# Performance work log

Measured on AMD Instinct MI355X. Metric: run time of the kernel, lower is better.

Reference implementation:

```python
import jax, jax.numpy as jnp
import numpy as np

BN_EPS = 1e-5
NUM_SUBSET = 3


def conv1x1(x, w, b):
    # x: [N, C, T, V], w: [O, C], b: [O]  (1x1 Conv2d)
    return jnp.einsum('nctv,oc->notv', x, w) + b[:, None, None]


def setup_inputs() -> dict:
    key = jax.random.key(0)
    ks = jax.random.split(key, 8)
    N, C, T, V = 64, 64, 300, 25
    IC = 16  # inter_c = out_channels // coff_embedding
    O = 64
    inp = {
        'x': jax.random.normal(ks[0], (N, C, T, V), dtype=jnp.float32),
        'A': jax.random.uniform(ks[1], (NUM_SUBSET, V, V), dtype=jnp.float32),
        'graph_attn': jnp.ones((NUM_SUBSET, V, V), dtype=jnp.float32),
        'g_w': jax.random.normal(ks[2], (NUM_SUBSET, O, C), dtype=jnp.float32) * 0.05,
        'g_b': jnp.zeros((NUM_SUBSET, O), dtype=jnp.float32),
        'a_w': jax.random.normal(ks[3], (NUM_SUBSET, IC, C), dtype=jnp.float32) * 0.05,
        'a_b': jnp.zeros((NUM_SUBSET, IC), dtype=jnp.float32),
        'b_w': jax.random.normal(ks[4], (NUM_SUBSET, IC, C), dtype=jnp.float32) * 0.05,
        'b_b': jnp.zeros((NUM_SUBSET, IC), dtype=jnp.float32),
        'bn_gamma': jnp.ones((O,), dtype=jnp.float32),
        'bn_beta': jnp.zeros((O,), dtype=jnp.float32),
        'bn_mean': jnp.zeros((O,), dtype=jnp.float32),
        'bn_var': jnp.ones((O,), dtype=jnp.float32),
    }
    return inp


def reference(x, A, graph_attn, g_w, g_b, a_w, a_b, b_w, b_b,
              bn_gamma, bn_beta, bn_mean, bn_var):
    N, C, T, V = x.shape
    IC = a_w.shape[1]
    A_tot = A + graph_attn  # [3, V, V]
    x_flat = x.reshape(N, C * T, V)
    hidden = None
    for i in range(NUM_SUBSET):
        # a_conv -> permute(0,3,1,2) -> [N, V, IC*T]
        A1 = conv1x1(x, a_w[i], a_b[i]).transpose(0, 3, 1, 2).reshape(N, V, IC * T)
        # b_conv -> [N, IC*T, V]
        A2 = conv1x1(x, b_w[i], b_b[i]).reshape(N, IC * T, V)
        attn = jax.nn.softmax(jnp.matmul(A1, A2) / (IC * T), axis=-2)  # [N, V, V], softmax over rows
        attn = attn + A_tot[i]
        z = jnp.matmul(x_flat, attn).reshape(N, C, T, V)
        z = conv1x1(z, g_w[i], g_b[i])
        hidden = z if hidden is None else hidden + z
    # BatchNorm2d in eval mode over channel dim
    inv = jax.lax.rsqrt(bn_var + BN_EPS)
    hidden = (hidden - bn_mean[:, None, None]) * (inv * bn_gamma)[:, None, None] + bn_beta[:, None, None]
    # in_channels == out_channels -> identity residual
    hidden = hidden + x
    return jax.nn.relu(hidden)
```

## Files before the change

kernel.cpp:

```cpp
#include <hip/hip_runtime.h>


#define NB 64
#define CB 64
#define TB 300
#define VB 25

typedef unsigned int uint32;
typedef unsigned short ushort16;
typedef __attribute__((ext_vector_type(8))) short short8;
typedef __attribute__((ext_vector_type(4))) float f32x4;
typedef __attribute__((ext_vector_type(16))) float f32x16;

__device__ __forceinline__ ushort16 f2bf(float f) {
    uint32 u = __float_as_uint(f);
    u = u + 0x7FFFu + ((u >> 16) & 1u);
    return (ushort16)(u >> 16);
}
__device__ __forceinline__ float bf2f(ushort16 h) {
    return __uint_as_float(((uint32)h) << 16);
}
__device__ __forceinline__ uint32 packbf2(float a, float b) {
    return (uint32)f2bf(a) | ((uint32)f2bf(b) << 16);
}

__global__ __launch_bounds__(256) void k1_attn_logits_mfma(
    const float* __restrict__ x, const float* __restrict__ a_w,
    const float* __restrict__ a_b, const float* __restrict__ b_w,
    const float* __restrict__ b_b, float* __restrict__ Mb)
{
    __shared__ ushort16 ws[96 * 64];
    __shared__ ushort16 xT[112 * 64];
    __shared__ ushort16 abT[192 * 64];
    __shared__ float    bias[96];

    const int tid   = threadIdx.x;
    const int n     = blockIdx.x / 25;
    const int chunk = blockIdx.x % 25;
    const float* xn = x + n * (CB * TB * VB);

    for (int idx = tid; idx < 6144; idx += 256) {
        int r = idx >> 6, c = idx & 63;
        float v = (r < 48) ? a_w[r * 64 + c] : b_w[(r - 48) * 64 + c];
        ws[r * 64 + ((((c >> 3) + r) & 7) << 3) + (c & 7)] = f2bf(v);
    }
    for (int idx = tid; idx < 96; idx += 256)
        bias[idx] = (idx < 48) ? a_b[idx] : b_b[idx - 48];

    const int w    = tid >> 6;
    const int lane = tid & 63;
    const int l15  = lane & 15;
    const int q    = lane >> 4;
    const int hi   = lane >> 5;
    const int v32  = lane & 31;

    f32x16 acc[3];
    #pragma unroll
    for (int i = 0; i < 3; ++i)
        #pragma unroll
        for (int r = 0; r < 16; ++r) acc[i][r] = 0.f;
    const f32x4 zf = (f32x4){0.f, 0.f, 0.f, 0.f};

    for (int s = 0; s < 3; ++s) {
        __syncthreads();
        const float* xs0 = xn + (chunk * 12 + s * 4) * 25;
        for (int idx = tid; idx < 1600; idx += 256) {
            int c = idx / 25, j = idx % 25;
            float4 v4 = *(const float4*)(xs0 + c * 7500 + j * 4);
            int tv0 = j * 4;
            #pragma unroll
            for (int e = 0; e < 4; ++e) {
                int tv = tv0 + e;
                float fv = (e == 0) ? v4.x : (e == 1) ? v4.y : (e == 2) ? v4.z : v4.w;
                xT[tv * 64 + ((((c >> 3) + tv) & 7) << 3) + (c & 7)] = f2bf(fv);
            }
        }
        __syncthreads();
        for (int tile = w; tile < 42; tile += 4) {
            int rt = tile / 7, ct = tile % 7;
            int r  = rt * 16 + l15;
            int tv = ct * 16 + l15;
            f32x4 d = zf;
            #pragma unroll
            for (int ss = 0; ss < 2; ++ss) {
                int kb = ss * 4 + q;
                short8 af = *(const short8*)&ws[r * 64 + (((kb + r) & 7) << 3)];
                short8 bf = *(const short8*)&xT[tv * 64 + (((kb + tv) & 7) << 3)];
                d = __builtin_amdgcn_mfma_f32_16x16x32_bf16(af, bf, d, 0, 0, 0);
            }
            if (tv < 100) {
                int tl = tv / 25, v = tv % 25;
                int r0 = rt * 16 + q * 4;
                float b0 = bias[r0], b1 = bias[r0 + 1];
                float b2 = bias[r0 + 2], b3 = bias[r0 + 3];
                int kb = tl * 2 + (q >> 1);
                uint32* dst = (uint32*)&abT[(rt * 32 + v) * 64 +
                                            (((kb + v) & 7) << 3) + ((q & 1) << 2)];
                dst[0] = packbf2(d[0] + b0, d[1] + b1);
                dst[1] = packbf2(d[2] + b2, d[3] + b3);
            }
        }
        __syncthreads();
        {
            int kb = w * 2 + hi;
            #pragma unroll
            for (int i = 0; i < 3; ++i) {
                short8 af = *(const short8*)&abT[(i * 32 + v32) * 64 +
                                                 (((kb + v32) & 7) << 3)];
                short8 bf = *(const short8*)&abT[((3 + i) * 32 + v32) * 64 +
                                                 (((kb + v32) & 7) << 3)];
                acc[i] = __builtin_amdgcn_mfma_f32_32x32x16_bf16(af, bf, acc[i], 0, 0, 0);
            }
        }
    }

    float* Ms = (float*)xT;
    __syncthreads();
    for (int idx = tid; idx < 3 * 32 * 33; idx += 256) Ms[idx] = 0.f;
    __syncthreads();
    for (int wv = 0; wv < 4; ++wv) {
        if (w == wv) {
            #pragma unroll
            for (int i = 0; i < 3; ++i)
                #pragma unroll
                for (int r = 0; r < 16; ++r) {
                    int row = (r & 3) + 8 * (r >> 2) + 4 * hi;
                    Ms[i * 1056 + row * 33 + v32] += acc[i][r];
                }
        }
        __syncthreads();
    }
    const float inv = 1.0f / 4800.0f;
    for (int idx = tid; idx < 1875; idx += 256) {
        int i = idx / 625, rem = idx % 625;
        int v1 = rem / 25, v2 = rem % 25;
        atomicAdd(Mb + ((i * NB + n) * 25 + v1) * 25 + v2,
                  Ms[i * 1056 + v1 * 33 + v2] * inv);
    }
}

__global__ __launch_bounds__(256) void k2_softmax_prep(
    const float* __restrict__ Mb, const float* __restrict__ A,
    const float* __restrict__ GA, const float* __restrict__ g_w,
    uint32* __restrict__ atT, uint32* __restrict__ gwb)
{
    int idx = blockIdx.x * 256 + threadIdx.x;
    if (idx < 4800) {
        int v2 = idx % 25, n = (idx / 25) % 64, i = idx / 1600;
        const float* mcol = Mb + ((i * 64 + n) * 25) * 25 + v2;
        float e[25], mx = -1e30f;
        #pragma unroll
        for (int v1 = 0; v1 < 25; ++v1) { e[v1] = mcol[v1 * 25]; mx = fmaxf(mx, e[v1]); }
        float s = 0.f;
        #pragma unroll
        for (int v1 = 0; v1 < 25; ++v1) { e[v1] = __expf(e[v1] - mx); s += e[v1]; }
        float invs = 1.0f / s;
        const float* acol = A + i * 625 + v2;
        const float* gcol = GA + i * 625 + v2;
        float w[25];
        #pragma unroll
        for (int v1 = 0; v1 < 25; ++v1)
            w[v1] = e[v1] * invs + acol[v1 * 25] + gcol[v1 * 25];
        uint32* row = atT + ((i * 64 + n) * 32 + v2) * 16;
        #pragma unroll
        for (int p = 0; p < 12; ++p) row[p] = packbf2(w[2 * p], w[2 * p + 1]);
        row[12] = (uint32)f2bf(w[24]);
        row[13] = 0u; row[14] = 0u; row[15] = 0u;
    } else if (idx < 4800 + 6144) {
        int j = idx - 4800;
        int o = j / 96, kp = j % 96;
        int k0 = 2 * kp;
        int i = k0 >> 6, c = k0 & 63;
        float lo = g_w[(i * 64 + o) * 64 + c];
        float hi = g_w[(i * 64 + o) * 64 + c + 1];
        gwb[o * 96 + kp] = packbf2(lo, hi);
    }
}

__global__ __launch_bounds__(256) void k3_out(
    const float* __restrict__ x, const uint32* __restrict__ atT,
    const ushort16* __restrict__ gwb, const float* __restrict__ g_b,
    const float* __restrict__ bn_g, const float* __restrict__ bn_b,
    const float* __restrict__ bn_m, const float* __restrict__ bn_v,
    float* __restrict__ out)
{
    __shared__ ushort16 xs[64 * 168];
    __shared__ uint32  xa[128 * 36];
    __shared__ uint32  ats[3 * 32 * 20];
    __shared__ float   bsc[64], bsh[64];

    const int tid = threadIdx.x;
    const int n  = blockIdx.x / 60;
    const int t0 = (blockIdx.x % 60) * 5;

    for (int idx = tid; idx < 8000; idx += 256) {
        int c = idx / 125, tv = idx % 125;
        int t = tv / 25, v = tv % 25;
        float g = x[((n * 64 + c) * 300 + t0 + t) * 25 + v];
        xs[c * 168 + t * 32 + v] = f2bf(g);
    }
    for (int idx = tid; idx < 64 * 35; idx += 256) {
        int c = idx / 35, r = idx % 35;
        xs[c * 168 + (r / 7) * 32 + 25 + (r % 7)] = (ushort16)0;
    }
    for (int idx = tid; idx < 1536; idx += 256) {
        int row = idx >> 4, d = idx & 15;
        ats[row * 20 + d] = atT[((row >> 5) * 64 + n) * 512 + (row & 31) * 16 + d];
    }
    for (int idx = tid; idx < 64; idx += 256) {
        float sc = bn_g[idx] * rsqrtf(bn_v[idx] + 1e-5f);
        bsc[idx] = sc;
        bsh[idx] = (g_b[idx] + g_b[64 + idx] + g_b[128 + idx] - bn_m[idx]) * sc + bn_b[idx];
    }
    for (int idx = tid; idx < 3 * 36; idx += 256)
        xa[(125 + idx / 36) * 36 + idx % 36] = 0u;

    const int w    = tid >> 6;
    const int lane = tid & 63;
    const int l15  = lane & 15;
    const int q    = lane >> 4;

    short8 gf[6];
    #pragma unroll
    for (int s = 0; s < 6; ++s)
        gf[s] = *(const short8*)(gwb + ((w * 16 + l15) * 192 + s * 32 + q * 8));

    f32x4 acc[8];
    #pragma unroll
    for (int ct = 0; ct < 8; ++ct) acc[ct] = (f32x4){0.f, 0.f, 0.f, 0.f};
    const f32x4 zf = (f32x4){0.f, 0.f, 0.f, 0.f};

    __syncthreads();

    for (int i = 0; i < 3; ++i) {
        if (i) __syncthreads();
        #pragma unroll
        for (int t = 0; t < 5; ++t) {
            short8 ax = *(const short8*)(xs + (w * 16 + l15) * 168 + t * 32 + q * 8);
            #pragma unroll
            for (int vt = 0; vt < 2; ++vt) {
                short8 bt = *(const short8*)((const ushort16*)ats +
                                             (i * 32 + vt * 16 + l15) * 40 + q * 8);
                f32x4 d = __builtin_amdgcn_mfma_f32_16x16x32_bf16(ax, bt, zf, 0, 0, 0);
                int v2 = vt * 16 + l15;
                if (v2 < 25) {
                    int col = t * 25 + v2;
                    int c0  = w * 16 + q * 4;
                    xa[col * 36 + (c0 >> 1)]     = packbf2(d[0], d[1]);
                    xa[col * 36 + (c0 >> 1) + 1] = packbf2(d[2], d[3]);
                }
            }
        }
        __syncthreads();
        #pragma unroll
        for (int ct = 0; ct < 8; ++ct) {
            #pragma unroll
            for (int s = 0; s < 2; ++s) {
                short8 bfrag = *(const short8*)((const ushort16*)xa +
                                                (ct * 16 + l15) * 72 + s * 32 + q * 8);
                acc[ct] = __builtin_amdgcn_mfma_f32_16x16x32_bf16(
                    gf[i * 2 + s], bfrag, acc[ct], 0, 0, 0);
            }
        }
    }

    const int o0 = w * 16 + q * 4;
    #pragma unroll
    for (int ct = 0; ct < 8; ++ct) {
        int col = ct * 16 + l15;
        if (col < 125) {
            int tl = col / 25;
            int v  = col - tl * 25;
            float* ob = out + (n * 64 + o0) * 7500 + t0 * 25 + col;
            #pragma unroll
            for (int r = 0; r < 4; ++r) {
                int o = o0 + r;
                float xv = bf2f(xs[o * 168 + tl * 32 + v]);
                float h = acc[ct][r] * bsc[o] + bsh[o] + xv;
                ob[r * 7500] = fmaxf(h, 0.f);
            }
        }
    }
}

extern "C" void kernel_launch(void* const* d_in, const int* in_sizes, int n_in,
                              void* d_out, int out_size, void* d_ws, size_t ws_size,
                              hipStream_t stream) {
    const float* x    = (const float*)d_in[0];
    const float* A    = (const float*)d_in[1];
    const float* GA   = (const float*)d_in[2];
    const float* g_w  = (const float*)d_in[3];
    const float* g_b  = (const float*)d_in[4];
    const float* a_w  = (const float*)d_in[5];
    const float* a_b  = (const float*)d_in[6];
    const float* b_w  = (const float*)d_in[7];
    const float* b_b  = (const float*)d_in[8];
    const float* bn_g = (const float*)d_in[9];
    const float* bn_b = (const float*)d_in[10];
    const float* bn_m = (const float*)d_in[11];
    const float* bn_v = (const float*)d_in[12];
    float* out = (float*)d_out;

    float*  Mb  = (float*)d_ws;
    uint32* atT = (uint32*)((char*)d_ws + 480000);
    uint32* gwb = (uint32*)((char*)d_ws + 480000 + 393216);

    hipMemsetAsync(d_ws, 0, 480000, stream);
    k1_attn_logits_mfma<<<dim3(1600), dim3(256), 0, stream>>>(x, a_w, a_b, b_w, b_b, Mb);
    k2_softmax_prep<<<dim3(43), dim3(256), 0, stream>>>(Mb, A, GA, g_w, atT, gwb);
    k3_out<<<dim3(3840), dim3(256), 0, stream>>>(x, atT, (const ushort16*)gwb,
                                                 g_b, bn_g, bn_b, bn_m, bn_v, out);
}
```

Baseline: 370.5 us.

## Split attention-logit MFMA by subset per wave and drop LDS reduction

In k1, each of three waves now owns one subset and accumulates all four time slices itself. Partial results go straight to global memory with atomics, so the LDS staging reduction and its serialized per-wave syncs are gone. The xT swizzle is changed to reduce LDS bank conflicts, and weight loading is vectorized to float2. k2 is restructured into one 64-thread block per (subset, batch) that stages the logits in LDS, plus vectorized g_w packing. One wave in k1 now idles during the logit MFMA phase, and more atomics hit global memory.

```diff
diff --git a/kernel.cpp b/kernel.cpp
--- a/kernel.cpp
+++ b/kernel.cpp
@@ -22,6 +22,10 @@
 }
 __device__ __forceinline__ uint32 packbf2(float a, float b) {
     return (uint32)f2bf(a) | ((uint32)f2bf(b) << 16);
+}
+
+__device__ __forceinline__ int xt_swz(int kb, int tv) {
+    return ((kb + tv + (tv >> 2)) & 7) << 3;
 }
 
 __global__ __launch_bounds__(256) void k1_attn_logits_mfma(
@@ -39,10 +43,13 @@
     const int chunk = blockIdx.x % 25;
     const float* xn = x + n * (CB * TB * VB);
 
-    for (int idx = tid; idx < 6144; idx += 256) {
-        int r = idx >> 6, c = idx & 63;
-        float v = (r < 48) ? a_w[r * 64 + c] : b_w[(r - 48) * 64 + c];
-        ws[r * 64 + ((((c >> 3) + r) & 7) << 3) + (c & 7)] = f2bf(v);
+    for (int idx = tid; idx < 3072; idx += 256) {
+        int r = idx >> 5, cp = idx & 31;
+        int c = cp * 2;
+        float2 v2 = (r < 48) ? *(const float2*)(a_w + r * 64 + c)
+                             : *(const float2*)(b_w + (r - 48) * 64 + c);
+        *(uint32*)&ws[r * 64 + ((((c >> 3) + r) & 7) << 3) + (c & 7)] =
+            packbf2(v2.x, v2.y);
     }
     for (int idx = tid; idx < 96; idx += 256)
         bias[idx] = (idx < 48) ? a_b[idx] : b_b[idx - 48];
@@ -54,11 +61,9 @@
     const int hi   = lane >> 5;
     const int v32  = lane & 31;
 
-    f32x16 acc[3];
+    f32x16 acc;
     #pragma unroll
-    for (int i = 0; i < 3; ++i)
-        #pragma unroll
-        for (int r = 0; r < 16; ++r) acc[i][r] = 0.f;
+    for (int r = 0; r < 16; ++r) acc[r] = 0.f;
     const f32x4 zf = (f32x4){0.f, 0.f, 0.f, 0.f};
 
     for (int s = 0; s < 3; ++s) {
@@ -72,7 +77,7 @@
             for (int e = 0; e < 4; ++e) {
                 int tv = tv0 + e;
                 float fv = (e == 0) ? v4.x : (e == 1) ? v4.y : (e == 2) ? v4.z : v4.w;
-                xT[tv * 64 + ((((c >> 3) + tv) & 7) << 3) + (c & 7)] = f2bf(fv);
+                xT[tv * 64 + xt_swz(c >> 3, tv) + (c & 7)] = f2bf(fv);
             }
         }
         __syncthreads();
@@ -85,7 +90,7 @@
             for (int ss = 0; ss < 2; ++ss) {
                 int kb = ss * 4 + q;
                 short8 af = *(const short8*)&ws[r * 64 + (((kb + r) & 7) << 3)];
-                short8 bf = *(const short8*)&xT[tv * 64 + (((kb + tv) & 7) << 3)];
+                short8 bf = *(const short8*)&xT[tv * 64 + xt_swz(kb, tv)];
                 d = __builtin_amdgcn_mfma_f32_16x16x32_bf16(af, bf, d, 0, 0, 0);
             }
             if (tv < 100) {
@@ -101,79 +106,77 @@
             }
         }
         __syncthreads();
-        {
-            int kb = w * 2 + hi;
-            #pragma unroll
-            for (int i = 0; i < 3; ++i) {
-                short8 af = *(const short8*)&abT[(i * 32 + v32) * 64 +
+        if (w < 3) {
+            #pragma unroll
+            for (int tl = 0; tl < 4; ++tl) {
+                int kb = tl * 2 + hi;
+                short8 af = *(const short8*)&abT[(w * 32 + v32) * 64 +
                                                  (((kb + v32) & 7) << 3)];
-                short8 bf = *(const short8*)&abT[((3 + i) * 32 + v32) * 64 +
+                short8 bf = *(const short8*)&abT[((3 + w) * 32 + v32) * 64 +
                                                  (((kb + v32) & 7) << 3)];
-                acc[i] = __builtin_amdgcn_mfma_f32_32x32x16_bf16(af, bf, acc[i], 0, 0, 0);
-            }
-        }
-    }
-
-    float* Ms = (float*)xT;
-    __syncthreads();
-    for (int idx = tid; idx < 3 * 32 * 33; idx += 256) Ms[idx] = 0.f;
-    __syncthreads();
-    for (int wv = 0; wv < 4; ++wv) {
-        if (w == wv) {
-            #pragma unroll
-            for (int i = 0; i < 3; ++i)
-                #pragma unroll
-                for (int r = 0; r < 16; ++r) {
-                    int row = (r & 3) + 8 * (r >> 2) + 4 * hi;
-                    Ms[i * 1056 + row * 33 + v32] += acc[i][r];
-                }
-        }
-        __syncthreads();
-    }
-    const float inv = 1.0f / 4800.0f;
-    for (int idx = tid; idx < 1875; idx += 256) {
-        int i = idx / 625, rem = idx % 625;
-        int v1 = rem / 25, v2 = rem % 25;
-        atomicAdd(Mb + ((i * NB + n) * 25 + v1) * 25 + v2,
-                  Ms[i * 1056 + v1 * 33 + v2] * inv);
-    }
-}
-
-__global__ __launch_bounds__(256) void k2_softmax_prep(
+                acc = __builtin_amdgcn_mfma_f32_32x32x16_bf16(af, bf, acc, 0, 0, 0);
+            }
+        }
+    }
+
+    if (w < 3 && v32 < 25) {
+        const float inv = 1.0f / 4800.0f;
+        #pragma unroll
+        for (int r = 0; r < 16; ++r) {
+            int row = (r & 3) + 8 * (r >> 2) + 4 * hi;
+            if (row < 25)
+                atomicAdd(Mb + ((w * NB + n) * 25 + row) * 25 + v32, acc[r] * inv);
+        }
+    }
+}
+
+__global__ __launch_bounds__(64) void k2_softmax_prep(
     const float* __restrict__ Mb, const float* __restrict__ A,
     const float* __restrict__ GA, const float* __restrict__ g_w,
     uint32* __restrict__ atT, uint32* __restrict__ gwb)
 {
-    int idx = blockIdx.x * 256 + threadIdx.x;
-    if (idx < 4800) {
-        int v2 = idx % 25, n = (idx / 25) % 64, i = idx / 1600;
-        const float* mcol = Mb + ((i * 64 + n) * 25) * 25 + v2;
-        float e[25], mx = -1e30f;
+    const int b   = blockIdx.x;
+    const int tid = threadIdx.x;
+    if (b < 192) {
+        __shared__ float Ms[640];
+        const int i = b >> 6, n = b & 63;
+        const float* src = Mb + b * 625;
+        for (int idx = tid; idx < 625; idx += 64) Ms[idx] = src[idx];
+        __syncthreads();
+        if (tid < 25) {
+            const int v2 = tid;
+            float e[25], mx = -1e30f;
+            #pragma unroll
+            for (int v1 = 0; v1 < 25; ++v1) {
+                e[v1] = Ms[v1 * 25 + v2];
+                mx = fmaxf(mx, e[v1]);
+            }
+            float s = 0.f;
+            #pragma unroll
+            for (int v1 = 0; v1 < 25; ++v1) { e[v1] = __expf(e[v1] - mx); s += e[v1]; }
+            float invs = 1.0f / s;
+            const float* acol = A + i * 625 + v2;
+            const float* gcol = GA + i * 625 + v2;
+            float wv[25];
+            #pragma unroll
+            for (int v1 = 0; v1 < 25; ++v1)
+                wv[v1] = e[v1] * invs + acol[v1 * 25] + gcol[v1 * 25];
+            uint32* row = atT + ((i * 64 + n) * 32 + v2) * 16;
+            #pragma unroll
+            for (int p = 0; p < 12; ++p) row[p] = packbf2(wv[2 * p], wv[2 * p + 1]);
+            row[12] = (uint32)f2bf(wv[24]);
+            row[13] = 0u; row[14] = 0u; row[15] = 0u;
+        }
+    } else {
+        int j0 = (b - 192) * 256 + tid * 4;
         #pragma unroll
-        for (int v1 = 0; v1 < 25; ++v1) { e[v1] = mcol[v1 * 25]; mx = fmaxf(mx, e[v1]); }
-        float s = 0.f;
-        #pragma unroll
-        for (int v1 = 0; v1 < 25; ++v1) { e[v1] = __expf(e[v1] - mx); s += e[v1]; }
-        float invs = 1.0f / s;
-        const float* acol = A + i * 625 + v2;
-        const float* gcol = GA + i * 625 + v2;
-        float w[25];
-        #pragma unroll
-        for (int v1 = 0; v1 < 25; ++v1)
-            w[v1] = e[v1] * invs + acol[v1 * 25] + gcol[v1 * 25];
-        uint32* row = atT + ((i * 64 + n) * 32 + v2) * 16;
-        #pragma unroll
-        for (int p = 0; p < 12; ++p) row[p] = packbf2(w[2 * p], w[2 * p + 1]);
-        row[12] = (uint32)f2bf(w[24]);
-        row[13] = 0u; row[14] = 0u; row[15] = 0u;
-    } else if (idx < 4800 + 6144) {
-        int j = idx - 4800;
-        int o = j / 96, kp = j % 96;
-        int k0 = 2 * kp;
-        int i = k0 >> 6, c = k0 & 63;
-        float lo = g_w[(i * 64 + o) * 64 + c];
-        float hi = g_w[(i * 64 + o) * 64 + c + 1];
-        gwb[o * 96 + kp] = packbf2(lo, hi);
+        for (int u = 0; u < 4; ++u) {
+            int j = j0 + u;
+            int o = j / 96, kp = j % 96;
+            int k0 = 2 * kp, i = k0 >> 6, c = k0 & 63;
+            float2 lh = *(const float2*)(g_w + (i * 64 + o) * 64 + c);
+            gwb[j] = packbf2(lh.x, lh.y);
+        }
     }
 }
 
@@ -307,7 +310,7 @@
 
     hipMemsetAsync(d_ws, 0, 480000, stream);
     k1_attn_logits_mfma<<<dim3(1600), dim3(256), 0, stream>>>(x, a_w, a_b, b_w, b_b, Mb);
-    k2_softmax_prep<<<dim3(43), dim3(256), 0, stream>>>(Mb, A, GA, g_w, atT, gwb);
+    k2_softmax_prep<<<dim3(216), dim3(64), 0, stream>>>(Mb, A, GA, g_w, atT, gwb);
     k3_out<<<dim3(3840), dim3(256), 0, stream>>>(x, atT, (const ushort16*)gwb,
                                                  g_b, bn_g, bn_b, bn_m, bn_v, out);
 }
```

Result: no change. 373.0 us (+0.7%).
